# Kernel optimization log

Hardware: AMD Instinct MI355X
Metric: run time of the kernel (lower is better)

The kernel has to match this reference:

```python
import jax, jax.numpy as jnp
import numpy as np

HEADS = 16
DIM_HEAD = 64
EPS = 1e-8


def setup_inputs() -> dict:
    key = jax.random.key(0)
    k1, k2, k3 = jax.random.split(key, 3)
    b, n, dim = 2, 2048, 1024
    inner = HEADS * DIM_HEAD
    x = jax.random.normal(k1, (b, n, dim), dtype=jnp.float32)
    mask = jnp.ones((b, n), dtype=bool)
    g = jnp.ones((dim,), dtype=jnp.float32)
    w_qkv = jax.random.normal(k2, (dim, inner * 3), dtype=jnp.float32) * (dim ** -0.5)
    w_out = jax.random.normal(k3, (inner, dim), dtype=jnp.float32) * (inner ** -0.5)
    return {"x": x, "mask": mask, "g": g, "w_qkv": w_qkv, "w_out": w_out}


def reference(x, mask, g, w_qkv, w_out):
    b, n, dim = x.shape
    scale = DIM_HEAD ** -0.5
    # RMSNorm: x / clamp(||x|| * dim^-0.5, eps) * g
    nrm = jnp.sqrt(jnp.sum(x * x, axis=-1, keepdims=True)) * (dim ** -0.5)
    xn = x / jnp.maximum(nrm, EPS) * g
    qkv = xn @ w_qkv  # [b, n, 3*inner]
    q, k, v = jnp.split(qkv, 3, axis=-1)

    def to_heads(t):  # b n (h d) -> b h n d
        return t.reshape(b, n, HEADS, DIM_HEAD).transpose(0, 2, 1, 3)

    q, k, v = to_heads(q) * scale, to_heads(k), to_heads(v)
    sim = jnp.einsum('bhid,bhjd->bhij', q, k)  # [b, h, n, n]
    max_neg = -jnp.finfo(sim.dtype).max
    sim = jnp.where(mask[:, None, None, :], sim, max_neg)
    causal = jnp.triu(jnp.ones((n, n), dtype=bool), 1)
    sim = jnp.where(causal, max_neg, sim)
    attn = jax.nn.softmax(sim, axis=-1)
    out = jnp.einsum('bhij,bhjd->bhid', attn, v)
    out = out.transpose(0, 2, 1, 3).reshape(b, n, HEADS * DIM_HEAD)
    return out @ w_out
```

## Files before the change

kernel.cpp:

```cpp
#include <hip/hip_runtime.h>
#include <hip/hip_bf16.h>
#include <math.h>

#define HEADS 16
#define DIMH  64
#define NSEQ  2048
#define BATCH 2
#define DIM   1024
#define INNER 1024

typedef __attribute__((ext_vector_type(4))) float f32x4;
typedef __attribute__((ext_vector_type(16))) float f32x16;
typedef __attribute__((ext_vector_type(8))) short s16x8;
typedef __attribute__((ext_vector_type(4))) unsigned int u32x4;
typedef unsigned int u32;

#define QSCALE 0.18033688011112042f

static __device__ __forceinline__ short f2bf(float f) {
    __hip_bfloat16 h = __float2bfloat16(f);
    return *reinterpret_cast<short*>(&h);
}

static __device__ __forceinline__ f32x4 mfma16(s16x8 a, s16x8 b, f32x4 c) {
    return __builtin_amdgcn_mfma_f32_16x16x32_bf16(a, b, c, 0, 0, 0);
}

static __device__ __forceinline__ f32x16 mfma32(s16x8 a, s16x8 b, f32x16 c) {
    return __builtin_amdgcn_mfma_f32_32x32x16_bf16(a, b, c, 0, 0, 0);
}

static __device__ __forceinline__ float exp2_fast(float x) {
    float r; asm("v_exp_f32 %0, %1" : "=v"(r) : "v"(x)); return r;
}

static __device__ __forceinline__ u32 cvtpk(float lo, float hi) {
    u32 r; asm("v_cvt_pk_bf16_f32 %0, %1, %2" : "=v"(r) : "v"(lo), "v"(hi));
    return r;
}

static __device__ __forceinline__ void gload16(const short* g, short* l) {
    __builtin_amdgcn_global_load_lds(
        (const __attribute__((address_space(1))) u32*)g,
        (__attribute__((address_space(3))) u32*)l, 16, 0, 0);
}

__global__ __launch_bounds__(256) void prep_k(const float* __restrict__ x,
                                              const float* __restrict__ g,
                                              short* __restrict__ xn,
                                              const float* __restrict__ wqkv,
                                              short* __restrict__ wqkvT,
                                              const float* __restrict__ wout,
                                              short* __restrict__ woutT) {
    int bx = blockIdx.x;
    if (bx < BATCH * NSEQ) {
        int row = bx;
        int t = threadIdx.x;
        const float4* xr = (const float4*)(x + (size_t)row * DIM);
        float4 v = xr[t];
        float ss = v.x * v.x + v.y * v.y + v.z * v.z + v.w * v.w;
#pragma unroll
        for (int m = 1; m < 64; m <<= 1) ss += __shfl_xor(ss, m);
        __shared__ float wss[4];
        int lane = t & 63, w = t >> 6;
        if (lane == 0) wss[w] = ss;
        __syncthreads();
        float tot = wss[0] + wss[1] + wss[2] + wss[3];
        float nrm = sqrtf(tot) * 0.03125f;
        float inv = 1.0f / fmaxf(nrm, 1e-8f);
        const float4* gr = (const float4*)g;
        float4 gv = gr[t];
        ushort4 o;
        o.x = (unsigned short)f2bf(v.x * inv * gv.x);
        o.y = (unsigned short)f2bf(v.y * inv * gv.y);
        o.z = (unsigned short)f2bf(v.z * inv * gv.z);
        o.w = (unsigned short)f2bf(v.w * inv * gv.w);
        *(ushort4*)(xn + (size_t)row * DIM + t * 4) = o;
    } else {
        int i = bx - BATCH * NSEQ;
        int tx128 = i & 127, ty32 = i >> 7;
        __shared__ float tile[32][33];
        const float* in;
        short* out;
        int C, R = DIM;
        int bc, br = ty32 * 32;
        if (tx128 < 96) { in = wqkv; out = wqkvT; C = 3 * INNER; bc = tx128 * 32; }
        else            { in = wout; out = woutT; C = DIM;       bc = (tx128 - 96) * 32; }
        int tx = threadIdx.x & 31, ty = threadIdx.x >> 5;
#pragma unroll
        for (int k = 0; k < 32; k += 8)
            tile[ty + k][tx] = in[(size_t)(br + ty + k) * C + bc + tx];
        __syncthreads();
#pragma unroll
        for (int k = 0; k < 32; k += 8)
            out[(size_t)(bc + ty + k) * R + br + tx] = f2bf(tile[tx][ty + k]);
    }
}

template <int EP>
__global__ __launch_bounds__(256) void gemm128_k(const short* __restrict__ A,
                                                 const short* __restrict__ Bt,
                                                 int M, int N, int K,
                                                 float* __restrict__ C,
                                                 short* __restrict__ qb,
                                                 short* __restrict__ kb,
                                                 short* __restrict__ vb) {
    __shared__ __align__(16) short As[128 * 32];
    __shared__ __align__(16) short Bs[128 * 32];
    int brow = blockIdx.y * 128, bcol = blockIdx.x * 128;
    int t = threadIdx.x, l = t & 63, w = t >> 6;
    int l15 = l & 15, lg = l >> 4;
    int wr = (w >> 1) * 64, wc = (w & 1) * 64;
    f32x4 acc[4][4] = {};
    int c0 = w * 64 + l;
    int c1 = 256 + w * 64 + l;
    int r0 = c0 >> 2, k0c = (c0 & 3) * 8;
    int r1 = c1 >> 2, k1c = (c1 & 3) * 8;
    const short* Ap0 = A + (size_t)(brow + r0) * K + k0c;
    const short* Ap1 = A + (size_t)(brow + r1) * K + k1c;
    const short* Bp0 = Bt + (size_t)(bcol + r0) * K + k0c;
    const short* Bp1 = Bt + (size_t)(bcol + r1) * K + k1c;
    for (int kk = 0; kk < K; kk += 32) {
        gload16(Ap0 + kk, &As[c0 * 8]);
        gload16(Ap1 + kk, &As[c1 * 8]);
        gload16(Bp0 + kk, &Bs[c0 * 8]);
        gload16(Bp1 + kk, &Bs[c1 * 8]);
        __syncthreads();
        s16x8 af[4], bf[4];
#pragma unroll
        for (int m = 0; m < 4; m++)
            af[m] = *(const s16x8*)&As[(wr + m * 16 + l15) * 32 + lg * 8];
#pragma unroll
        for (int n = 0; n < 4; n++)
            bf[n] = *(const s16x8*)&Bs[(wc + n * 16 + l15) * 32 + lg * 8];
#pragma unroll
        for (int m = 0; m < 4; m++)
#pragma unroll
            for (int n = 0; n < 4; n++)
                acc[m][n] = mfma16(af[m], bf[n], acc[m][n]);
        __syncthreads();
    }
#pragma unroll
    for (int m = 0; m < 4; m++)
#pragma unroll
        for (int n = 0; n < 4; n++)
#pragma unroll
            for (int r = 0; r < 4; r++) {
                int row = brow + wr + m * 16 + lg * 4 + r;
                int col = bcol + wc + n * 16 + l15;
                float val = acc[m][n][r];
                if (EP == 0) {
                    int which = col >> 10;
                    int ic = col & 1023;
                    int h = ic >> 6, d = ic & 63;
                    int b = row >> 11, nr = row & 2047;
                    size_t off = ((((size_t)b * HEADS + h) * NSEQ) + nr) * DIMH + d;
                    float sv = (which == 0) ? val * QSCALE : val;
                    short o = f2bf(sv);
                    if (which == 0) qb[off] = o;
                    else if (which == 1) kb[off] = o;
                    else vb[off] = o;
                } else {
                    C[(size_t)row * N + col] = val;
                }
            }
}

__global__ __launch_bounds__(256) void gemm_n64_k(const short* __restrict__ A,
                                                  const short* __restrict__ Bt,
                                                  int M, int N, int K,
                                                  float* __restrict__ C) {
    __shared__ __align__(16) short As[128 * 32];
    __shared__ __align__(16) short Bs[64 * 32];
    int brow = blockIdx.y * 128, bcol = blockIdx.x * 64;
    int t = threadIdx.x, l = t & 63, w = t >> 6;
    int l15 = l & 15, lg = l >> 4;
    int wr = (w >> 1) * 64, wc = (w & 1) * 32;
    f32x4 acc[4][2] = {};
    int c0 = w * 64 + l;
    int c1 = 256 + c0;
    int r0 = c0 >> 2, k0c = (c0 & 3) * 8;
    int r1 = c1 >> 2, k1c = (c1 & 3) * 8;
    const short* Ap0 = A + (size_t)(brow + r0) * K + k0c;
    const short* Ap1 = A + (size_t)(brow + r1) * K + k1c;
    const short* Bp0 = Bt + (size_t)(bcol + r0) * K + k0c;
    for (int kk = 0; kk < K; kk += 32) {
        gload16(Ap0 + kk, &As[c0 * 8]);
        gload16(Ap1 + kk, &As[c1 * 8]);
        gload16(Bp0 + kk, &Bs[c0 * 8]);
        __syncthreads();
        s16x8 af[4], bf[2];
#pragma unroll
        for (int m = 0; m < 4; m++)
            af[m] = *(const s16x8*)&As[(wr + m * 16 + l15) * 32 + lg * 8];
#pragma unroll
        for (int n = 0; n < 2; n++)
            bf[n] = *(const s16x8*)&Bs[(wc + n * 16 + l15) * 32 + lg * 8];
#pragma unroll
        for (int m = 0; m < 4; m++)
#pragma unroll
            for (int n = 0; n < 2; n++)
                acc[m][n] = mfma16(af[m], bf[n], acc[m][n]);
        __syncthreads();
    }
#pragma unroll
    for (int m = 0; m < 4; m++)
#pragma unroll
        for (int n = 0; n < 2; n++)
#pragma unroll
            for (int r = 0; r < 4; r++) {
                int row = brow + wr + m * 16 + lg * 4 + r;
                int col = bcol + wc + n * 16 + l15;
                C[(size_t)row * N + col] = acc[m][n][r];
            }
}

__global__ __launch_bounds__(256) void attn_k(const short* __restrict__ Q,
                                              const short* __restrict__ K,
                                              const short* __restrict__ V,
                                              short* __restrict__ O) {
    __shared__ __align__(16) short Kd[2][64][72];
    __shared__ __align__(16) short Vt[2][64][72];
    __shared__ __align__(16) u32 Ot[4][32 * 36];
    int bh = blockIdx.y;
    int qi = blockIdx.x;
    int qt = (bh < 16) ? qi : 15 - qi;
    int b = bh >> 4, h = bh & 15;
    const short* Qp = Q + (size_t)bh * NSEQ * DIMH;
    const short* Kp = K + (size_t)bh * NSEQ * DIMH;
    const short* Vp = V + (size_t)bh * NSEQ * DIMH;
    int t = threadIdx.x, lane = t & 63, w = t >> 6;
    int l31 = lane & 31, hh = lane >> 5;
    int qbase = qt * 128;
    int qg = qbase + w * 32 + l31;
    s16x8 qfr[4];
#pragma unroll
    for (int ks = 0; ks < 4; ks++)
        qfr[ks] = *(const s16x8*)(Qp + (size_t)qg * DIMH + ks * 16 + hh * 8);
    float mrow = -INFINITY, lsum = 0.f;
    f32x16 acc0 = {}, acc1 = {};
    int jend = qbase + 128;
    int kr = lane, kd0 = w * 16;
    s16x8 nk0, nk1, nv0, nv1;

#define STAGE_LOAD(JB) {                                                    \
        const short* kp_ = Kp + (size_t)((JB) + kr) * DIMH + kd0;           \
        const short* vp_ = Vp + (size_t)((JB) + kr) * DIMH + kd0;           \
        nk0 = *(const s16x8*)kp_; nk1 = *(const s16x8*)(kp_ + 8);           \
        nv0 = *(const s16x8*)vp_; nv1 = *(const s16x8*)(vp_ + 8); }

#define STAGE_WRITE(NB) {                                                   \
        *(s16x8*)&Kd[NB][kr][kd0] = nk0;                                    \
        *(s16x8*)&Kd[NB][kr][kd0 + 8] = nk1;                                \
        _Pragma("unroll")                                                   \
        for (int e = 0; e < 8; e++) {                                       \
            Vt[NB][kd0 + e][kr] = nv0[e];                                   \
            Vt[NB][kd0 + 8 + e][kr] = nv1[e];                               \
        } }

    STAGE_LOAD(0);
    STAGE_WRITE(0);
    __syncthreads();
    int cur = 0;
    for (int jb = 0; jb < jend; jb += 64) {
        bool hn = (jb + 64) < jend;
        if (hn) STAGE_LOAD(jb + 64);
        bool active = (jb <= qbase + w * 32 + 31);
        f32x16 sa0 = {}, sa1 = {};
        u32 pkw0[8], pkw1[8];
        if (active) {
            __builtin_amdgcn_s_setprio(1);
#pragma unroll
            for (int ks = 0; ks < 4; ks++) {
                s16x8 kf0 = *(const s16x8*)&Kd[cur][l31][ks * 16 + hh * 8];
                s16x8 kf1 = *(const s16x8*)&Kd[cur][32 + l31][ks * 16 + hh * 8];
                sa0 = mfma32(kf0, qfr[ks], sa0);
                sa1 = mfma32(kf1, qfr[ks], sa1);
            }
            __builtin_amdgcn_s_setprio(0);
            if (jb + 63 > qbase + w * 32) {
#pragma unroll
                for (int r = 0; r < 16; r++) {
                    int jo = (r & 3) + 8 * (r >> 2) + 4 * hh;
                    if (jb + jo > qg) sa0[r] = -INFINITY;
                    if (jb + 32 + jo > qg) sa1[r] = -INFINITY;
                }
            }
            float pmc[4] = {-INFINITY, -INFINITY, -INFINITY, -INFINITY};
#pragma unroll
            for (int r = 0; r < 16; r += 4) {
#pragma unroll
                for (int u = 0; u < 4; u++)
                    pmc[u] = fmaxf(pmc[u], fmaxf(sa0[r + u], sa1[r + u]));
            }
            float pm = fmaxf(fmaxf(pmc[0], pmc[1]), fmaxf(pmc[2], pmc[3]));
            pm = fmaxf(pm, __shfl_xor(pm, 32));
            if (!__all(pm - mrow <= 8.0f)) {
                float mn = fmaxf(mrow, pm);
                float sc = exp2_fast(mrow - mn);
                mrow = mn;
                lsum *= sc;
#pragma unroll
                for (int r = 0; r < 16; r++) { acc0[r] *= sc; acc1[r] *= sc; }
            }
            float psc[4] = {0.f, 0.f, 0.f, 0.f};
#pragma unroll
            for (int r = 0; r < 16; r += 4) {
#pragma unroll
                for (int u = 0; u < 4; u++) {
                    sa0[r + u] = exp2_fast(sa0[r + u] - mrow);
                    sa1[r + u] = exp2_fast(sa1[r + u] - mrow);
                    psc[u] += sa0[r + u] + sa1[r + u];
                }
            }
            float ps = (psc[0] + psc[1]) + (psc[2] + psc[3]);
            ps += __shfl_xor(ps, 32);
            lsum += ps;
#pragma unroll
            for (int r2 = 0; r2 < 8; r2++) {
                pkw0[r2] = cvtpk(sa0[2 * r2], sa0[2 * r2 + 1]);
                pkw1[r2] = cvtpk(sa1[2 * r2], sa1[2 * r2 + 1]);
            }
        }
        if (hn) STAGE_WRITE(cur ^ 1);
        if (active) {
#pragma unroll
            for (int ks = 0; ks < 4; ks++) {
                const u32* pw = (ks < 2) ? pkw0 : pkw1;
                int a = (ks & 1) * 4;
                u32 e0 = hh ? pw[a] : pw[a + 2];
                u32 e1 = hh ? pw[a + 1] : pw[a + 3];
                u32 t0 = (u32)__shfl_xor((int)e0, 32);
                u32 t1 = (u32)__shfl_xor((int)e1, 32);
                u32x4 wd;
                wd[0] = hh ? t0 : pw[a];
                wd[1] = hh ? t1 : pw[a + 1];
                wd[2] = hh ? pw[a + 2] : t0;
                wd[3] = hh ? pw[a + 3] : t1;
                s16x8 pf = *(s16x8*)&wd;
                s16x8 vf0 = *(const s16x8*)&Vt[cur][l31][ks * 16 + hh * 8];
                s16x8 vf1 = *(const s16x8*)&Vt[cur][32 + l31][ks * 16 + hh * 8];
                __builtin_amdgcn_s_setprio(1);
                acc0 = mfma32(vf0, pf, acc0);
                acc1 = mfma32(vf1, pf, acc1);
                __builtin_amdgcn_s_setprio(0);
            }
        }
        if (hn) __syncthreads();
        cur ^= 1;
    }
    float inv = 1.0f / lsum;
    u32* myOt = &Ot[w][0];
#pragma unroll
    for (int g = 0; g < 4; g++) {
        u32 w00 = cvtpk(acc0[4 * g] * inv, acc0[4 * g + 1] * inv);
        u32 w01 = cvtpk(acc0[4 * g + 2] * inv, acc0[4 * g + 3] * inv);
        u32 w10 = cvtpk(acc1[4 * g] * inv, acc1[4 * g + 1] * inv);
        u32 w11 = cvtpk(acc1[4 * g + 2] * inv, acc1[4 * g + 3] * inv);
        int c0 = 4 * g + 2 * hh;
        myOt[l31 * 36 + c0] = w00;
        myOt[l31 * 36 + c0 + 1] = w01;
        myOt[l31 * 36 + 16 + c0] = w10;
        myOt[l31 * 36 + 16 + c0 + 1] = w11;
    }
    int q2 = lane >> 1, c2 = (lane & 1) * 16;
    short* op = O + (size_t)(b * NSEQ + qbase + w * 32 + q2) * INNER
              + h * DIMH + c2 * 2;
#pragma unroll
    for (int i = 0; i < 4; i++) {
        u32x4 ov = *(const u32x4*)&myOt[q2 * 36 + c2 + 4 * i];
        *(u32x4*)(op + 8 * i) = ov;
    }
#undef STAGE_LOAD
#undef STAGE_WRITE
}

extern "C" void kernel_launch(void* const* d_in, const int* in_sizes, int n_in,
                              void* d_out, int out_size, void* d_ws, size_t ws_size,
                              hipStream_t stream) {
    const float* x     = (const float*)d_in[0];
    const float* g     = (const float*)d_in[2];
    const float* w_qkv = (const float*)d_in[3];
    const float* w_out = (const float*)d_in[4];
    float* out = (float*)d_out;

    char* ws = (char*)d_ws;
    short* xn    = (short*)(ws);
    short* wqkvT = (short*)(ws + (size_t)(8  << 20));
    short* woutT = (short*)(ws + (size_t)(14 << 20));
    short* qb    = (short*)(ws + (size_t)(16 << 20));
    short* kb    = (short*)(ws + (size_t)(24 << 20));
    short* vb    = (short*)(ws + (size_t)(32 << 20));
    short* ao    = (short*)(ws + (size_t)(40 << 20));

    prep_k<<<dim3(BATCH * NSEQ + 4096), dim3(256), 0, stream>>>(
        x, g, xn, w_qkv, wqkvT, w_out, woutT);
    gemm128_k<0><<<dim3(3 * INNER / 128, BATCH * NSEQ / 128), dim3(256), 0, stream>>>(
        xn, wqkvT, BATCH * NSEQ, 3 * INNER, DIM, nullptr, qb, kb, vb);
    attn_k<<<dim3(NSEQ / 128, BATCH * HEADS), dim3(256), 0, stream>>>(qb, kb, vb, ao);
    gemm_n64_k<<<dim3(DIM / 64, BATCH * NSEQ / 128), dim3(256), 0, stream>>>(
        ao, woutT, BATCH * NSEQ, DIM, INNER, out);
}
```

Measured before the change: 136.9 us.

## Deepen K/V prefetch to two tiles ahead with unrolled ping-pong registers

The attention loop is unrolled by two, with two sets of prefetch registers (A and B) so global loads for K/V tiles are issued two iterations ahead of use rather than one. LDS writes of the next tile now happen after the whole compute of the current tile instead of between QK and PV. This gives global loads more latency cover and removes the mid-compute LDS store. The cost is higher register pressure and a larger unrolled body.

After: 124.6 us. 9.0% less time.

```diff
diff --git a/kernel.cpp b/kernel.cpp
--- a/kernel.cpp
+++ b/kernel.cpp
@@ -240,114 +240,137 @@
     float mrow = -INFINITY, lsum = 0.f;
     f32x16 acc0 = {}, acc1 = {};
     int jend = qbase + 128;
+    int nt = jend >> 6;
     int kr = lane, kd0 = w * 16;
-    s16x8 nk0, nk1, nv0, nv1;
-
-#define STAGE_LOAD(JB) {                                                    \
+    s16x8 ak0, ak1, av0, av1;
+    s16x8 bk0, bk1, bv0, bv1;
+
+#define LOADA(JB) {                                                         \
         const short* kp_ = Kp + (size_t)((JB) + kr) * DIMH + kd0;           \
         const short* vp_ = Vp + (size_t)((JB) + kr) * DIMH + kd0;           \
-        nk0 = *(const s16x8*)kp_; nk1 = *(const s16x8*)(kp_ + 8);           \
-        nv0 = *(const s16x8*)vp_; nv1 = *(const s16x8*)(vp_ + 8); }
-
-#define STAGE_WRITE(NB) {                                                   \
-        *(s16x8*)&Kd[NB][kr][kd0] = nk0;                                    \
-        *(s16x8*)&Kd[NB][kr][kd0 + 8] = nk1;                                \
+        ak0 = *(const s16x8*)kp_; ak1 = *(const s16x8*)(kp_ + 8);           \
+        av0 = *(const s16x8*)vp_; av1 = *(const s16x8*)(vp_ + 8); }
+#define LOADB(JB) {                                                         \
+        const short* kp_ = Kp + (size_t)((JB) + kr) * DIMH + kd0;           \
+        const short* vp_ = Vp + (size_t)((JB) + kr) * DIMH + kd0;           \
+        bk0 = *(const s16x8*)kp_; bk1 = *(const s16x8*)(kp_ + 8);           \
+        bv0 = *(const s16x8*)vp_; bv1 = *(const s16x8*)(vp_ + 8); }
+#define WRITEA(NB) {                                                        \
+        *(s16x8*)&Kd[NB][kr][kd0] = ak0;                                    \
+        *(s16x8*)&Kd[NB][kr][kd0 + 8] = ak1;                                \
         _Pragma("unroll")                                                   \
         for (int e = 0; e < 8; e++) {                                       \
-            Vt[NB][kd0 + e][kr] = nv0[e];                                   \
-            Vt[NB][kd0 + 8 + e][kr] = nv1[e];                               \
+            Vt[NB][kd0 + e][kr] = av0[e];                                   \
+            Vt[NB][kd0 + 8 + e][kr] = av1[e];                               \
         } }
-
-    STAGE_LOAD(0);
-    STAGE_WRITE(0);
+#define WRITEB(NB) {                                                        \
+        *(s16x8*)&Kd[NB][kr][kd0] = bk0;                                    \
+        *(s16x8*)&Kd[NB][kr][kd0 + 8] = bk1;                                \
+        _Pragma("unroll")                                                   \
+        for (int e = 0; e < 8; e++) {                                       \
+            Vt[NB][kd0 + e][kr] = bv0[e];                                   \
+            Vt[NB][kd0 + 8 + e][kr] = bv1[e];                               \
+        } }
+
+#define COMPUTE(CUR, JB) {                                                  \
+        bool active = ((JB) <= qbase + w * 32 + 31);                        \
+        if (active) {                                                       \
+            f32x16 sa0 = {}, sa1 = {};                                      \
+            __builtin_amdgcn_s_setprio(1);                                  \
+            _Pragma("unroll")                                               \
+            for (int ks = 0; ks < 4; ks++) {                                \
+                s16x8 kf0 = *(const s16x8*)&Kd[CUR][l31][ks * 16 + hh * 8]; \
+                s16x8 kf1 = *(const s16x8*)&Kd[CUR][32 + l31][ks * 16 + hh * 8]; \
+                sa0 = mfma32(kf0, qfr[ks], sa0);                            \
+                sa1 = mfma32(kf1, qfr[ks], sa1);                            \
+            }                                                               \
+            __builtin_amdgcn_s_setprio(0);                                  \
+            if ((JB) + 63 > qbase + w * 32) {                               \
+                _Pragma("unroll")                                           \
+                for (int r = 0; r < 16; r++) {                              \
+                    int jo = (r & 3) + 8 * (r >> 2) + 4 * hh;               \
+                    if ((JB) + jo > qg) sa0[r] = -INFINITY;                 \
+                    if ((JB) + 32 + jo > qg) sa1[r] = -INFINITY;            \
+                }                                                           \
+            }                                                               \
+            float pmc[4] = {-INFINITY, -INFINITY, -INFINITY, -INFINITY};    \
+            _Pragma("unroll")                                               \
+            for (int r = 0; r < 16; r += 4) {                               \
+                _Pragma("unroll")                                           \
+                for (int u = 0; u < 4; u++)                                 \
+                    pmc[u] = fmaxf(pmc[u], fmaxf(sa0[r + u], sa1[r + u]));  \
+            }                                                               \
+            float pm = fmaxf(fmaxf(pmc[0], pmc[1]), fmaxf(pmc[2], pmc[3])); \
+            pm = fmaxf(pm, __shfl_xor(pm, 32));                             \
+            if (!__all(pm - mrow <= 8.0f)) {                                \
+                float mn = fmaxf(mrow, pm);                                 \
+                float sc = exp2_fast(mrow - mn);                            \
+                mrow = mn;                                                  \
+                lsum *= sc;                                                 \
+                _Pragma("unroll")                                           \
+                for (int r = 0; r < 16; r++) { acc0[r] *= sc; acc1[r] *= sc; } \
+            }                                                               \
+            float psc[4] = {0.f, 0.f, 0.f, 0.f};                            \
+            _Pragma("unroll")                                               \
+            for (int r = 0; r < 16; r += 4) {                               \
+                _Pragma("unroll")                                           \
+                for (int u = 0; u < 4; u++) {                               \
+                    sa0[r + u] = exp2_fast(sa0[r + u] - mrow);              \
+                    sa1[r + u] = exp2_fast(sa1[r + u] - mrow);              \
+                    psc[u] += sa0[r + u] + sa1[r + u];                      \
+                }                                                           \
+            }                                                               \
+            float ps = (psc[0] + psc[1]) + (psc[2] + psc[3]);               \
+            ps += __shfl_xor(ps, 32);                                       \
+            lsum += ps;                                                     \
+            u32 pkw0[8], pkw1[8];                                           \
+            _Pragma("unroll")                                               \
+            for (int r2 = 0; r2 < 8; r2++) {                                \
+                pkw0[r2] = cvtpk(sa0[2 * r2], sa0[2 * r2 + 1]);             \
+                pkw1[r2] = cvtpk(sa1[2 * r2], sa1[2 * r2 + 1]);             \
+            }                                                               \
+            _Pragma("unroll")                                               \
+            for (int ks = 0; ks < 4; ks++) {                                \
+                const u32* pw = (ks < 2) ? pkw0 : pkw1;                     \
+                int a = (ks & 1) * 4;                                       \
+                u32 e0 = hh ? pw[a] : pw[a + 2];                            \
+                u32 e1 = hh ? pw[a + 1] : pw[a + 3];                        \
+                u32 t0 = (u32)__shfl_xor((int)e0, 32);                      \
+                u32 t1 = (u32)__shfl_xor((int)e1, 32);                      \
+                u32x4 wd;                                                   \
+                wd[0] = hh ? t0 : pw[a];                                    \
+                wd[1] = hh ? t1 : pw[a + 1];                                \
+                wd[2] = hh ? pw[a + 2] : t0;                                \
+                wd[3] = hh ? pw[a + 3] : t1;                                \
+                s16x8 pf = *(s16x8*)&wd;                                    \
+                s16x8 vf0 = *(const s16x8*)&Vt[CUR][l31][ks * 16 + hh * 8]; \
+                s16x8 vf1 = *(const s16x8*)&Vt[CUR][32 + l31][ks * 16 + hh * 8]; \
+                __builtin_amdgcn_s_setprio(1);                              \
+                acc0 = mfma32(vf0, pf, acc0);                               \
+                acc1 = mfma32(vf1, pf, acc1);                               \
+                __builtin_amdgcn_s_setprio(0);                              \
+            }                                                               \
+        }                                                                   \
+    }
+
+    LOADA(0);
+    WRITEA(0);
+    LOADB(64);
     __syncthreads();
-    int cur = 0;
-    for (int jb = 0; jb < jend; jb += 64) {
-        bool hn = (jb + 64) < jend;
-        if (hn) STAGE_LOAD(jb + 64);
-        bool active = (jb <= qbase + w * 32 + 31);
-        f32x16 sa0 = {}, sa1 = {};
-        u32 pkw0[8], pkw1[8];
-        if (active) {
-            __builtin_amdgcn_s_setprio(1);
-#pragma unroll
-            for (int ks = 0; ks < 4; ks++) {
-                s16x8 kf0 = *(const s16x8*)&Kd[cur][l31][ks * 16 + hh * 8];
-                s16x8 kf1 = *(const s16x8*)&Kd[cur][32 + l31][ks * 16 + hh * 8];
-                sa0 = mfma32(kf0, qfr[ks], sa0);
-                sa1 = mfma32(kf1, qfr[ks], sa1);
-            }
-            __builtin_amdgcn_s_setprio(0);
-            if (jb + 63 > qbase + w * 32) {
-#pragma unroll
-                for (int r = 0; r < 16; r++) {
-                    int jo = (r & 3) + 8 * (r >> 2) + 4 * hh;
-                    if (jb + jo > qg) sa0[r] = -INFINITY;
-                    if (jb + 32 + jo > qg) sa1[r] = -INFINITY;
-                }
-            }
-            float pmc[4] = {-INFINITY, -INFINITY, -INFINITY, -INFINITY};
-#pragma unroll
-            for (int r = 0; r < 16; r += 4) {
-#pragma unroll
-                for (int u = 0; u < 4; u++)
-                    pmc[u] = fmaxf(pmc[u], fmaxf(sa0[r + u], sa1[r + u]));
-            }
-            float pm = fmaxf(fmaxf(pmc[0], pmc[1]), fmaxf(pmc[2], pmc[3]));
-            pm = fmaxf(pm, __shfl_xor(pm, 32));
-            if (!__all(pm - mrow <= 8.0f)) {
-                float mn = fmaxf(mrow, pm);
-                float sc = exp2_fast(mrow - mn);
-                mrow = mn;
-                lsum *= sc;
-#pragma unroll
-                for (int r = 0; r < 16; r++) { acc0[r] *= sc; acc1[r] *= sc; }
-            }
-            float psc[4] = {0.f, 0.f, 0.f, 0.f};
-#pragma unroll
-            for (int r = 0; r < 16; r += 4) {
-#pragma unroll
-                for (int u = 0; u < 4; u++) {
-                    sa0[r + u] = exp2_fast(sa0[r + u] - mrow);
-                    sa1[r + u] = exp2_fast(sa1[r + u] - mrow);
-                    psc[u] += sa0[r + u] + sa1[r + u];
-                }
-            }
-            float ps = (psc[0] + psc[1]) + (psc[2] + psc[3]);
-            ps += __shfl_xor(ps, 32);
-            lsum += ps;
-#pragma unroll
-            for (int r2 = 0; r2 < 8; r2++) {
-                pkw0[r2] = cvtpk(sa0[2 * r2], sa0[2 * r2 + 1]);
-                pkw1[r2] = cvtpk(sa1[2 * r2], sa1[2 * r2 + 1]);
-            }
+    for (int p = 0; p < nt; p += 2) {
+        int jb0 = p * 64, jb1 = jb0 + 64;
+        bool h2 = (p + 2) < nt;
+        bool h3 = (p + 3) < nt;
+        if (h2) LOADA(jb0 + 128);
+        COMPUTE(0, jb0);
+        WRITEB(1);
+        __syncthreads();
+        if (h3) LOADB(jb1 + 128);
+        COMPUTE(1, jb1);
+        if (h2) {
+            WRITEA(0);
+            __syncthreads();
         }
-        if (hn) STAGE_WRITE(cur ^ 1);
-        if (active) {
-#pragma unroll
-            for (int ks = 0; ks < 4; ks++) {
-                const u32* pw = (ks < 2) ? pkw0 : pkw1;
-                int a = (ks & 1) * 4;
-                u32 e0 = hh ? pw[a] : pw[a + 2];
-                u32 e1 = hh ? pw[a + 1] : pw[a + 3];
-                u32 t0 = (u32)__shfl_xor((int)e0, 32);
-                u32 t1 = (u32)__shfl_xor((int)e1, 32);
-                u32x4 wd;
-                wd[0] = hh ? t0 : pw[a];
-                wd[1] = hh ? t1 : pw[a + 1];
-                wd[2] = hh ? pw[a + 2] : t0;
-                wd[3] = hh ? pw[a + 3] : t1;
-                s16x8 pf = *(s16x8*)&wd;
-                s16x8 vf0 = *(const s16x8*)&Vt[cur][l31][ks * 16 + hh * 8];
-                s16x8 vf1 = *(const s16x8*)&Vt[cur][32 + l31][ks * 16 + hh * 8];
-                __builtin_amdgcn_s_setprio(1);
-                acc0 = mfma32(vf0, pf, acc0);
-                acc1 = mfma32(vf1, pf, acc1);
-                __builtin_amdgcn_s_setprio(0);
-            }
-        }
-        if (hn) __syncthreads();
-        cur ^= 1;
     }
     float inv = 1.0f / lsum;
     u32* myOt = &Ot[w][0];
@@ -371,8 +394,11 @@
         u32x4 ov = *(const u32x4*)&myOt[q2 * 36 + c2 + 4 * i];
         *(u32x4*)(op + 8 * i) = ov;
     }
-#undef STAGE_LOAD
-#undef STAGE_WRITE
+#undef LOADA
+#undef LOADB
+#undef WRITEA
+#undef WRITEB
+#undef COMPUTE
 }
 
 extern "C" void kernel_launch(void* const* d_in, const int* in_sizes, int n_in,
```
